# Kernel optimization log

Hardware: AMD Instinct MI355X
Metric: run time of the kernel (lower is better)

Reference implementation:

```python
import jax, jax.numpy as jnp
import numpy as np

B, T, D, I, C, H = 8192, 128, 7, 128, 10, 64
L = 2 ** D
SUBSET = int(I * 0.8)  # feature_subset_size = 102


def setup_inputs() -> dict:
    key = jax.random.key(0)
    ks = jax.random.split(key, 7)
    x = jax.random.normal(ks[0], (B, I), dtype=jnp.float32)
    # exact feature-subset mask: SUBSET ones per (tree, depth) row
    r = jax.random.uniform(ks[1], (T, D, I))
    ranks = jnp.argsort(jnp.argsort(r, axis=-1), axis=-1)
    feature_mask = (ranks < SUBSET).astype(jnp.float32)
    thresholds = jax.random.normal(ks[2], (T, D), dtype=jnp.float32)
    leaf_outputs = jax.random.normal(ks[3], (T, L, C), dtype=jnp.float32)
    W1 = jax.random.normal(ks[4], (I, H), dtype=jnp.float32) * 0.08
    b1 = jnp.zeros((H,), dtype=jnp.float32)
    W2 = jax.random.normal(ks[5], (H, T), dtype=jnp.float32) * 0.12
    b2 = jnp.zeros((T,), dtype=jnp.float32)
    return {"x": x, "feature_mask": feature_mask, "thresholds": thresholds,
            "leaf_outputs": leaf_outputs, "W1": W1, "b1": b1, "W2": W2, "b2": b2}


def reference(x, feature_mask, thresholds, leaf_outputs, W1, b1, W2, b2):
    depth = thresholds.shape[1]
    # split logits: masked feature sum minus threshold, per (batch, tree, depth)
    z = jnp.einsum('bi,tdi->btd', x, feature_mask) - thresholds[None, :, :]
    s = 0.5 * (z / (1.0 + jnp.abs(z)) + 1.0)  # scaled softsign split in (0,1)
    # probabilistic path routing: doubling concat, identical to torch loop
    p = jnp.ones((x.shape[0], feature_mask.shape[0], 1), dtype=x.dtype)
    for d in range(depth):
        sd = s[:, :, d:d + 1]            # [B, T, 1]
        p = jnp.concatenate([p * sd, p * (1.0 - sd)], axis=-1)  # [B, T, 2^(d+1)]
    leaf_probs = jax.nn.softmax(leaf_outputs, axis=-1)           # [T, L, C]
    tree_outputs = jnp.einsum('btl,tlc->btc', p, leaf_probs)     # [B, T, C]
    # instance-wise attention over trees (eval mode: no dropout)
    attn = jax.nn.softmax(jax.nn.relu(x @ W1 + b1) @ W2 + b2, axis=-1)  # [B, T]
    return jnp.sum(tree_outputs * attn[:, :, None], axis=1)     # [B, C]
```

## Files before the change

### kernel.cpp

```cpp
#include <hip/hip_runtime.h>
#include <hip/hip_bf16.h>
#include <hip/hip_fp16.h>


#define BB 8192
#define TT 128
#define II 128
#define CC 10
#define HH 64

#define OFF_LPB 524288
#define OFF_XBF 606208
#define OFF_MBF 1130496

typedef __attribute__((ext_vector_type(8))) short short8;
typedef __attribute__((ext_vector_type(16))) float floatx16;

static __device__ inline unsigned int pkbf(float lo, float hi) {
  __hip_bfloat162 h = __float22bfloat162_rn(make_float2(lo, hi));
  unsigned int u;
  __builtin_memcpy(&u, &h, 4);
  return u;
}

static __device__ inline unsigned int pkh(float lo, float hi) {
  __half2 h = __float22half2_rn(make_float2(lo, hi));
  unsigned int u;
  __builtin_memcpy(&u, &h, 4);
  return u;
}

static __device__ inline short8 cvt8(float4 a, float4 b) {
  union { short8 v; unsigned int u[4]; } r;
  r.u[0] = pkbf(a.x, a.y);
  r.u[1] = pkbf(a.z, a.w);
  r.u[2] = pkbf(b.x, b.y);
  r.u[3] = pkbf(b.z, b.w);
  return r.v;
}

__global__ __launch_bounds__(64) void prep_kernel(
    const float* __restrict__ x, const float* __restrict__ mask,
    const float* __restrict__ lo,
    const float* __restrict__ W1, const float* __restrict__ b1,
    const float* __restrict__ W2, const float* __restrict__ b2,
    __half* __restrict__ attnB, unsigned int* __restrict__ lpbG,
    unsigned short* __restrict__ xbf, unsigned short* __restrict__ mbf,
    float* __restrict__ out) {
  __shared__ __align__(16) char smem_raw[6144];
  const int blk = blockIdx.x;
  const int lane = threadIdx.x;
  const int half = lane >> 5, l31 = lane & 31;

  if (blk < 256) {
    const int b0 = blk * 32;

    short8 axf[8];
    const float* xrow = x + (size_t)(b0 + l31) * II + half * 8;
#pragma unroll
    for (int s = 0; s < 8; ++s)
      axf[s] = cvt8(*(const float4*)(xrow + s * 16),
                    *(const float4*)(xrow + s * 16 + 4));

    floatx16 acch[2];
#pragma unroll
    for (int i = 0; i < 16; ++i) { acch[0][i] = 0.f; acch[1][i] = 0.f; }
#pragma unroll
    for (int s = 0; s < 8; ++s) {
#pragma unroll
      for (int tile = 0; tile < 2; ++tile) {
        union { short8 v; unsigned int u[4]; } wf;
#pragma unroll
        for (int jp = 0; jp < 4; ++jp) {
          int k0 = s * 16 + half * 8 + jp * 2;
          float f0 = W1[(size_t)k0 * HH + tile * 32 + l31];
          float f1 = W1[(size_t)(k0 + 1) * HH + tile * 32 + l31];
          wf.u[jp] = pkbf(f0, f1);
        }
        acch[tile] = __builtin_amdgcn_mfma_f32_32x32x16_bf16(
            axf[s], wf.v, acch[tile], 0, 0, 0);
      }
    }
    __hip_bfloat16* hids = (__hip_bfloat16*)smem_raw;
#pragma unroll
    for (int tile = 0; tile < 2; ++tile) {
      float bh = b1[tile * 32 + l31];
#pragma unroll
      for (int r = 0; r < 16; ++r) {
        int row = (r & 3) + 8 * (r >> 2) + 4 * half;
        hids[row * 72 + tile * 32 + l31] =
            __float2bfloat16(fmaxf(acch[tile][r] + bh, 0.f));
      }
    }
    __syncthreads();

    short8 ahf[4];
#pragma unroll
    for (int s = 0; s < 4; ++s)
      ahf[s] = *(const short8*)(hids + l31 * 72 + s * 16 + half * 8);

    floatx16 accl[4];
#pragma unroll
    for (int tile = 0; tile < 4; ++tile) {
#pragma unroll
      for (int i = 0; i < 16; ++i) accl[tile][i] = 0.f;
#pragma unroll
      for (int s = 0; s < 4; ++s) {
        union { short8 v; unsigned int u[4]; } wf;
#pragma unroll
        for (int jp = 0; jp < 4; ++jp) {
          int k0 = s * 16 + half * 8 + jp * 2;
          float f0 = W2[(size_t)k0 * TT + tile * 32 + l31];
          float f1 = W2[(size_t)(k0 + 1) * TT + tile * 32 + l31];
          wf.u[jp] = pkbf(f0, f1);
        }
        accl[tile] = __builtin_amdgcn_mfma_f32_32x32x16_bf16(
            ahf[s], wf.v, accl[tile], 0, 0, 0);
      }
      float bt = b2[tile * 32 + l31];
#pragma unroll
      for (int i = 0; i < 16; ++i) accl[tile][i] += bt;
    }

    float mrow[16];
#pragma unroll
    for (int r = 0; r < 16; ++r)
      mrow[r] = fmaxf(fmaxf(accl[0][r], accl[1][r]),
                      fmaxf(accl[2][r], accl[3][r]));
#pragma unroll
    for (int msk = 1; msk <= 16; msk <<= 1)
#pragma unroll
      for (int r = 0; r < 16; ++r)
        mrow[r] = fmaxf(mrow[r], __shfl_xor(mrow[r], msk, 64));
    float srow[16];
#pragma unroll
    for (int r = 0; r < 16; ++r) srow[r] = 0.f;
#pragma unroll
    for (int tile = 0; tile < 4; ++tile)
#pragma unroll
      for (int r = 0; r < 16; ++r) {
        float e = __expf(accl[tile][r] - mrow[r]);
        accl[tile][r] = e;
        srow[r] += e;
      }
#pragma unroll
    for (int msk = 1; msk <= 16; msk <<= 1)
#pragma unroll
      for (int r = 0; r < 16; ++r)
        srow[r] += __shfl_xor(srow[r], msk, 64);
#pragma unroll
    for (int r = 0; r < 16; ++r) srow[r] = 1.f / srow[r];

#pragma unroll
    for (int tile = 0; tile < 4; ++tile)
#pragma unroll
      for (int r = 0; r < 16; ++r) {
        int row = (r & 3) + 8 * (r >> 2) + 4 * half;
        attnB[(size_t)(b0 + row) * TT + tile * 32 + l31] =
            __float2half(accl[tile][r] * srow[r]);
      }

  } else if (blk < 384) {
    float* lps = (float*)smem_raw;
    const int t0 = blk - 256;
#pragma unroll
    for (int rr = 0; rr < 2; ++rr) {
      int l = lane * 2 + rr;
      const float* row = lo + ((size_t)t0 * 128 + l) * CC;
      float v[CC];
      float m = -1e30f;
#pragma unroll
      for (int c = 0; c < CC; ++c) { v[c] = row[c]; m = fmaxf(m, v[c]); }
      float s = 0.f;
#pragma unroll
      for (int c = 0; c < CC; ++c) { v[c] = __expf(v[c] - m); s += v[c]; }
      float inv = 1.f / s;
      float* o = lps + l * 12;
#pragma unroll
      for (int c = 0; c < CC; ++c) o[c] = v[c] * inv;
    }
    __syncthreads();

#pragma unroll
    for (int jj = 0; jj < 3; ++jj) {
      int idx = jj * 64 + lane;
      if (idx < 160) {
        int s = idx / 20, e = idx - s * 20;
        int n = e >> 1, hf = e & 1;
        unsigned int wd[4];
#pragma unroll
        for (int jp = 0; jp < 4; ++jp) {
          int l0 = s * 16 + hf * 8 + jp * 2;
          float f0 = lps[l0 * 12 + n];
          float f1 = lps[(l0 + 1) * 12 + n];
          wd[jp] = pkh(f0, f1);
        }
        ((uint4*)lpbG)[(size_t)t0 * 160 + idx] =
            make_uint4(wd[0], wd[1], wd[2], wd[3]);
      }
    }
  } else if (blk < 668) {
    const float* src;
    unsigned short* dst;
    size_t base;
    if (blk < 640) { src = x;    dst = xbf; base = (size_t)(blk - 384) * 4096; }
    else           { src = mask; dst = mbf; base = (size_t)(blk - 640) * 4096; }
#pragma unroll
    for (int j = 0; j < 8; ++j) {
      size_t e = base + (size_t)j * 512 + (size_t)lane * 8;
      float4 a = *(const float4*)(src + e);
      float4 b = *(const float4*)(src + e + 4);
      *(short8*)(dst + e) = cvt8(a, b);
    }
  } else {
    const int base4 = (blk - 668) * 512;
#pragma unroll
    for (int j = 0; j < 8; ++j)
      ((float4*)out)[base4 + j * 64 + lane] = make_float4(0.f, 0.f, 0.f, 0.f);
  }
}

__global__ __launch_bounds__(256, 6) void main_kernel(
    const unsigned short* __restrict__ xbf, const unsigned short* __restrict__ mbf,
    const float* __restrict__ thr, const __half* __restrict__ attnB,
    const unsigned int* __restrict__ lpbG, float* __restrict__ out) {
  __shared__ __align__(16) char smem_raw[18432];
  const int tid = threadIdx.x;
  const int wv = tid >> 6, lane = tid & 63;
  const int half = lane >> 5, l31 = lane & 31;
  const int phys = blockIdx.x;
  const int bg2 = (phys & 7) * 8 + (phys >> 8);
  const int tg4 = (phys >> 3) & 31;
  const int bl = wv * 32 + l31;

  __half* zsl = (__half*)smem_raw;
  uint4* st4 = (uint4*)(smem_raw + 8192);

  const uint4* lpg = (const uint4*)lpbG + (size_t)tg4 * 640;
  uint4 stg0 = lpg[wv * 64 + lane];
  uint4 stg1 = lpg[(wv + 4) * 64 + lane];
  uint4 stg2 = make_uint4(0u, 0u, 0u, 0u);
  if (wv < 2) stg2 = lpg[(wv + 8) * 64 + lane];

  __half av[4];
  *(uint2*)av = ((const uint2*)attnB)[(size_t)(bg2 * 128 + bl) * 32 + tg4];

  {
    const int m0 = tg4 * 28;
    short8 xf[8];
    const unsigned short* xr = xbf + (size_t)(bg2 * 128 + bl) * II + half * 8;
#pragma unroll
    for (int s = 0; s < 8; ++s) xf[s] = *(const short8*)(xr + s * 16);

    int mr = m0 + l31; if (mr > 895) mr = 895;
    const unsigned short* mrow = mbf + (size_t)mr * II + half * 8;

    floatx16 acc;
#pragma unroll
    for (int i = 0; i < 16; ++i) acc[i] = 0.f;
#pragma unroll
    for (int s = 0; s < 8; ++s) {
      short8 af = *(const short8*)(mrow + s * 16);
      acc = __builtin_amdgcn_mfma_f32_32x32x16_bf16(af, xf[s], acc, 0, 0, 0);
    }

#pragma unroll
    for (int r = 0; r < 16; ++r) {
      int row = (r & 3) + 8 * (r >> 2) + 4 * half;
      if (row < 28) {
        int tl = row / 7;
        int d = row - tl * 7;
        float z = acc[r] - thr[m0 + row];
        float o = 0.5f * (z / (1.f + fabsf(z)) + 1.f);
        zsl[((tl * 128) + bl) * 8 + d] = __float2half(o);
      }
    }
  }

  st4[wv * 64 + lane] = stg0;
  st4[(wv + 4) * 64 + lane] = stg1;
  if (wv < 2) st4[(wv + 8) * 64 + lane] = stg2;
  __syncthreads();

  {
    const uint4* zsl4 = (const uint4*)smem_raw;

    floatx16 acc;
#pragma unroll
    for (int i = 0; i < 16; ++i) acc[i] = 0.f;

#pragma unroll
    for (int it = 0; it < 4; ++it) {
      uint4 bf[8];
#pragma unroll
      for (int s = 0; s < 8; ++s)
        bf[s] = (l31 < CC) ? st4[(it * 8 + s) * 20 + l31 * 2 + half]
                           : make_uint4(0u, 0u, 0u, 0u);
      uint4 sv = zsl4[it * 128 + bl];

      const __half* sh = (const __half*)&sv;
      float s0 = __half2float(sh[0]), s1 = __half2float(sh[1]);
      float s2 = __half2float(sh[2]), s3 = __half2float(sh[3]);
      float s4 = __half2float(sh[4]), s5 = __half2float(sh[5]);
      float s6 = __half2float(sh[6]);
      float A  = __half2float(av[it]);

      float s0c = 1.f - s0, s1c = 1.f - s1, s2c = 1.f - s2;
      float t0 = s0 * s1, t1 = s0c * s1, t2 = s0 * s1c, t3 = s0c * s1c;
      float pl[8];
      pl[0] = t0 * s2;  pl[1] = t1 * s2;  pl[2] = t2 * s2;  pl[3] = t3 * s2;
      pl[4] = t0 * s2c; pl[5] = t1 * s2c; pl[6] = t2 * s2c; pl[7] = t3 * s2c;
      float sel3 = half ? (1.f - s3) : s3;
      float Af = A * sel3;
      float s4c = 1.f - s4, s5c = 1.f - s5;
      float as6 = Af * s6, as6c = Af * (1.f - s6);
      float u0 = s4 * s5, u1 = s4c * s5, u2 = s4 * s5c, u3 = s4c * s5c;
      float wv8[8];
      wv8[0] = u0 * as6;  wv8[1] = u1 * as6;
      wv8[2] = u2 * as6;  wv8[3] = u3 * as6;
      wv8[4] = u0 * as6c; wv8[5] = u1 * as6c;
      wv8[6] = u2 * as6c; wv8[7] = u3 * as6c;
      __half2 pl2[4];
#pragma unroll
      for (int jp = 0; jp < 4; ++jp)
        pl2[jp] = __float22half2_rn(make_float2(pl[jp * 2], pl[jp * 2 + 1]));

#pragma unroll
      for (int s = 0; s < 8; ++s) {
        union { short8 v; __half2 h[4]; } a0;
        __half2 w2 = __half2half2(__float2half(wv8[s]));
#pragma unroll
        for (int jp = 0; jp < 4; ++jp) a0.h[jp] = __hmul2(pl2[jp], w2);
        acc = __builtin_amdgcn_mfma_f32_32x32x16_f16(
            a0.v, *(const short8*)&bf[s], acc, 0, 0, 0);
      }
    }

    __syncthreads();
    float* red = (float*)smem_raw;
    if (l31 < CC) {
#pragma unroll
      for (int r = 0; r < 16; ++r) {
        int row = (r & 3) + 8 * (r >> 2) + 4 * half;
        red[(wv * 32 + row) * 10 + l31] = acc[r];
      }
    }
    __syncthreads();
#pragma unroll
    for (int j = 0; j < 5; ++j) {
      int idx = tid + 256 * j;
      atomicAdd(out + (size_t)bg2 * 1280 + idx, red[idx]);
    }
  }
}

extern "C" void kernel_launch(void* const* d_in, const int* in_sizes, int n_in,
                              void* d_out, int out_size, void* d_ws, size_t ws_size,
                              hipStream_t stream) {
  const float* x    = (const float*)d_in[0];
  const float* mask = (const float*)d_in[1];
  const float* thr  = (const float*)d_in[2];
  const float* lo   = (const float*)d_in[3];
  const float* W1   = (const float*)d_in[4];
  const float* b1   = (const float*)d_in[5];
  const float* W2   = (const float*)d_in[6];
  const float* b2   = (const float*)d_in[7];
  float* out = (float*)d_out;
  float* ws  = (float*)d_ws;

  __half*         attnB = (__half*)ws;
  unsigned int*   LPb   = (unsigned int*)(ws + OFF_LPB);
  unsigned short* xbf   = (unsigned short*)(ws + OFF_XBF);
  unsigned short* mbf   = (unsigned short*)(ws + OFF_MBF);

  prep_kernel<<<708, 64, 0, stream>>>(x, mask, lo, W1, b1, W2, b2,
                                      attnB, LPb, xbf, mbf, out);
  main_kernel<<<2048, 256, 0, stream>>>(xbf, mbf, thr, attnB, LPb, out);
}
```

Measured before the change: 106.7 us.

## Load leaf-prob tiles directly from global with register double-buffering, drop LDS staging

Leaf-probability B-operands are no longer staged through shared memory with a block barrier. Each wave now reads them straight from global memory into two register buffers, prefetching the next step while the current MFMA step runs. This shrinks LDS use, which lets launch bounds rise from 6 to 8 blocks per CU, and the block-index mapping is reordered so blocks on the same XCD share batch groups. The risks are more global and L2 traffic, since each block rereads the tiles with mostly idle lanes, and higher register pressure from the double buffers.

```diff
diff --git a/kernel.cpp b/kernel.cpp
--- a/kernel.cpp
+++ b/kernel.cpp
@@ -220,33 +220,27 @@
   }
 }
 
-__global__ __launch_bounds__(256, 6) void main_kernel(
+__global__ __launch_bounds__(256, 8) void main_kernel(
     const unsigned short* __restrict__ xbf, const unsigned short* __restrict__ mbf,
     const float* __restrict__ thr, const __half* __restrict__ attnB,
     const unsigned int* __restrict__ lpbG, float* __restrict__ out) {
-  __shared__ __align__(16) char smem_raw[18432];
+  __shared__ __align__(16) char smem_raw[8192];
   const int tid = threadIdx.x;
   const int wv = tid >> 6, lane = tid & 63;
   const int half = lane >> 5, l31 = lane & 31;
   const int phys = blockIdx.x;
-  const int bg2 = (phys & 7) * 8 + (phys >> 8);
-  const int tg4 = (phys >> 3) & 31;
+  const int xcd = phys & 7;
+  const int bg2 = xcd * 8 + ((phys >> 3) & 7);
+  const int tg8 = phys >> 6;
   const int bl = wv * 32 + l31;
 
   __half* zsl = (__half*)smem_raw;
-  uint4* st4 = (uint4*)(smem_raw + 8192);
-
-  const uint4* lpg = (const uint4*)lpbG + (size_t)tg4 * 640;
-  uint4 stg0 = lpg[wv * 64 + lane];
-  uint4 stg1 = lpg[(wv + 4) * 64 + lane];
-  uint4 stg2 = make_uint4(0u, 0u, 0u, 0u);
-  if (wv < 2) stg2 = lpg[(wv + 8) * 64 + lane];
 
   __half av[4];
-  *(uint2*)av = ((const uint2*)attnB)[(size_t)(bg2 * 128 + bl) * 32 + tg4];
+  *(uint2*)av = ((const uint2*)attnB)[(size_t)(bg2 * 128 + bl) * 32 + tg8];
 
   {
-    const int m0 = tg4 * 28;
+    const int m0 = tg8 * 28;
     short8 xf[8];
     const unsigned short* xr = xbf + (size_t)(bg2 * 128 + bl) * II + half * 8;
 #pragma unroll
@@ -277,27 +271,16 @@
     }
   }
 
-  st4[wv * 64 + lane] = stg0;
-  st4[(wv + 4) * 64 + lane] = stg1;
-  if (wv < 2) st4[(wv + 8) * 64 + lane] = stg2;
-  __syncthreads();
-
   {
     const uint4* zsl4 = (const uint4*)smem_raw;
+    const uint4* lpt = (const uint4*)lpbG + (size_t)tg8 * 640;
 
     floatx16 acc;
 #pragma unroll
     for (int i = 0; i < 16; ++i) acc[i] = 0.f;
 
-#pragma unroll
-    for (int it = 0; it < 4; ++it) {
-      uint4 bf[8];
-#pragma unroll
-      for (int s = 0; s < 8; ++s)
-        bf[s] = (l31 < CC) ? st4[(it * 8 + s) * 20 + l31 * 2 + half]
-                           : make_uint4(0u, 0u, 0u, 0u);
+    auto dostep = [&](int it, const uint4* bf) {
       uint4 sv = zsl4[it * 128 + bl];
-
       const __half* sh = (const __half*)&sv;
       float s0 = __half2float(sh[0]), s1 = __half2float(sh[1]);
       float s2 = __half2float(sh[2]), s3 = __half2float(sh[3]);
@@ -334,7 +317,24 @@
         acc = __builtin_amdgcn_mfma_f32_32x32x16_f16(
             a0.v, *(const short8*)&bf[s], acc, 0, 0, 0);
       }
-    }
+    };
+
+#define PF(dst, itn)                                                       \
+  _Pragma("unroll") for (int s = 0; s < 8; ++s)                            \
+      dst[s] = (l31 < CC) ? lpt[((itn) * 8 + s) * 20 + l31 * 2 + half]     \
+                          : make_uint4(0u, 0u, 0u, 0u);
+
+    uint4 bf0[8], bf1[8];
+    PF(bf0, 0)
+#pragma unroll
+    for (int ith = 0; ith < 2; ++ith) {
+      const int it = ith * 2;
+      PF(bf1, it + 1)
+      dostep(it, bf0);
+      if (ith < 1) { PF(bf0, it + 2) }
+      dostep(it + 1, bf1);
+    }
+#undef PF
 
     __syncthreads();
     float* red = (float*)smem_raw;
```

After: 166.2 us. +55.8%, slower.
